# Kernel tuning notes

Hardware: AMD Instinct MI355X
Metric: run time of the kernel (lower is better)

## Reference

```python
import jax, jax.numpy as jnp
import numpy as np

N = 50000
E = 800000
IN_C = 512
HID = 256
OUT_C = 2
NUM_LAYERS = 3
NUM_HIER = 3
EPS = 1e-5


def setup_inputs() -> dict:
    key = jax.random.key(0)
    ks = jax.random.split(key, 24)
    g = lambda k, shp, fan: jax.random.normal(k, shp, jnp.float32) / np.sqrt(fan)
    inp = {
        "x": jax.random.normal(ks[0], (N, IN_C), jnp.float32),
        "edge_index": jax.random.randint(ks[1], (2, E), 0, N, jnp.int64),
        # GCN conv weights/biases
        "conv_w0": g(ks[2], (IN_C, HID), IN_C),
        "conv_ws": g(ks[3], (NUM_LAYERS - 1, HID, HID), HID),
        "conv_b": jnp.zeros((NUM_LAYERS, HID), jnp.float32),
        "bn_g": jnp.ones((NUM_LAYERS, HID), jnp.float32),
        "bn_b": jnp.zeros((NUM_LAYERS, HID), jnp.float32),
        # global-path MLPs
        "fcg_w0": g(ks[4], (HID, HID), HID),
        "fcg_ws": g(ks[5], (NUM_HIER - 1, 2 * HID, HID), 2 * HID),
        "fcg_b": jnp.zeros((NUM_HIER, HID), jnp.float32),
        "bng_g": jnp.ones((NUM_HIER, HID), jnp.float32),
        "bng_b": jnp.zeros((NUM_HIER, HID), jnp.float32),
        # local-path MLPs
        "fcl_w": g(ks[6], (NUM_HIER, HID, HID), HID),
        "fcl_b": jnp.zeros((NUM_HIER, HID), jnp.float32),
        "bnl_g": jnp.ones((NUM_HIER, HID), jnp.float32),
        "bnl_b": jnp.zeros((NUM_HIER, HID), jnp.float32),
        # output heads
        "outg_w": g(ks[7], (HID, OUT_C), HID),
        "outg_b": jnp.zeros((OUT_C,), jnp.float32),
        "outl_w": g(ks[8], (NUM_HIER, HID, OUT_C), HID),
        "outl_b": jnp.zeros((NUM_HIER, OUT_C), jnp.float32),
    }
    return inp


def _gcn_edges(edge_index):
    # add self-loops, compute symmetric normalization D^-1/2 (A+I) D^-1/2
    loops = jnp.arange(N, dtype=edge_index.dtype)
    rows = jnp.concatenate([edge_index[0], loops])
    cols = jnp.concatenate([edge_index[1], loops])
    deg = jax.ops.segment_sum(jnp.ones_like(rows, jnp.float32), rows, num_segments=N)
    dinv = jnp.where(deg > 0, jax.lax.rsqrt(deg), 0.0)
    w = dinv[rows] * dinv[cols]
    return rows, cols, w


def _propagate(h, rows, cols, w):
    msg = h[cols] * w[:, None]          # [E+N, HID] gather
    return jax.ops.segment_sum(msg, rows, num_segments=N)


def _bn(h, gamma, beta):
    m = h.mean(0)
    v = h.var(0)
    return gamma * (h - m) * jax.lax.rsqrt(v + EPS) + beta


def reference(x, edge_index, conv_w0, conv_ws, conv_b, bn_g, bn_b,
              fcg_w0, fcg_ws, fcg_b, bng_g, bng_b,
              fcl_w, fcl_b, bnl_g, bnl_b,
              outg_w, outg_b, outl_w, outl_b):
    rows, cols, ew = _gcn_edges(edge_index)
    h = x
    for i in range(NUM_LAYERS):
        W = conv_w0 if i == 0 else conv_ws[i - 1]
        h = _propagate(h @ W, rows, cols, ew) + conv_b[i]
        h = jax.nn.relu(_bn(h, bn_g[i], bn_b[i]))  # dropout = identity (eval)
    # hierarchical global path
    hg = []
    xg = jax.nn.relu(_bn(h @ fcg_w0 + fcg_b[0], bng_g[0], bng_b[0]))
    hg.append(xg)
    for i in range(NUM_HIER - 1):
        xg = jnp.concatenate([hg[i], h], -1) @ fcg_ws[i] + fcg_b[i + 1]
        xg = jax.nn.relu(_bn(xg, bng_g[i + 1], bng_b[i + 1]))
        hg.append(xg)
    og = jax.nn.log_softmax(hg[-1] @ outg_w + outg_b, axis=-1)
    # local heads
    ol = []
    for i in range(NUM_HIER):
        hl = jax.nn.relu(_bn(hg[i] @ fcl_w[i] + fcl_b[i], bnl_g[i], bnl_b[i]))
        ol.append(jax.nn.log_softmax(hl @ outl_w[i] + outl_b[i], axis=-1))
    # stack: [1 + NUM_HIER, N, OUT_C] (og first, then local heads)
    return jnp.stack([og] + ol, axis=0)
```

## Files before the change

### kernel.cpp

```cpp
#include <hip/hip_runtime.h>
#include <math.h>

#define N_NODES 50000
#define E_EDGES 800000
#define HID 256
#define EPS_BN 1e-5f

typedef __attribute__((ext_vector_type(8))) short short8;
typedef __attribute__((ext_vector_type(4))) float floatx4;
typedef __attribute__((ext_vector_type(8))) unsigned short ushort8v;

__device__ __forceinline__ unsigned short f2bf(float f) {
    unsigned u = __float_as_uint(f);
    u = (u + 0x7FFFu + ((u >> 16) & 1u)) >> 16;
    return (unsigned short)u;
}
__device__ __forceinline__ float bf2f(unsigned short b) {
    return __uint_as_float(((unsigned)b) << 16);
}

__global__ __launch_bounds__(256) void k_deg(const int* __restrict__ rows,
                                             int* __restrict__ deg) {
    int e = blockIdx.x * 256 + threadIdx.x;
    atomicAdd(&deg[rows[e]], 1);
}

__global__ __launch_bounds__(256) void k_dinv(const int* __restrict__ deg,
                                              float* __restrict__ dinv) {
    int n = blockIdx.x * 256 + threadIdx.x;
    if (n < N_NODES) dinv[n] = rsqrtf((float)deg[n] + 1.0f);
}

__global__ __launch_bounds__(1024) void k_scan(const int* __restrict__ deg,
                                               int* __restrict__ rowptr) {
    __shared__ int wsum[16];
    __shared__ int carry_s;
    int tid = threadIdx.x, lane = tid & 63, w = tid >> 6;
    if (tid == 0) carry_s = 0;
    __syncthreads();
    for (int base = 0; base < N_NODES; base += 1024) {
        int v = (base + tid < N_NODES) ? deg[base + tid] : 0;
        int x = v;
#pragma unroll
        for (int d = 1; d < 64; d <<= 1) {
            int t = __shfl_up(x, d);
            if (lane >= d) x += t;
        }
        if (lane == 63) wsum[w] = x;
        __syncthreads();
        if (w == 0) {
            int ws = (lane < 16) ? wsum[lane] : 0;
#pragma unroll
            for (int d = 1; d < 16; d <<= 1) {
                int t = __shfl_up(ws, d);
                if (lane >= d) ws += t;
            }
            if (lane < 16) wsum[lane] = ws;
        }
        __syncthreads();
        int c = carry_s;
        int wbase = (w > 0) ? wsum[w - 1] : 0;
        if (base + tid < N_NODES) rowptr[base + tid] = c + wbase + x - v;
        __syncthreads();
        if (tid == 0) carry_s = c + wsum[15];
        __syncthreads();
    }
    if (threadIdx.x == 0) rowptr[N_NODES] = carry_s;
}

__global__ __launch_bounds__(256) void k_fill(const int* __restrict__ rows,
                                              const int* __restrict__ cols,
                                              const int* __restrict__ rowptr,
                                              int* __restrict__ cursor,
                                              int* __restrict__ colidx) {
    int e = blockIdx.x * 256 + threadIdx.x;
    int r = rows[e];
    int pos = atomicAdd(&cursor[r], 1);
    colidx[rowptr[r] + pos] = cols[e];
}

__global__ __launch_bounds__(256) void k_f2bf_vec(const float* __restrict__ X,
                                                  unsigned short* __restrict__ Y,
                                                  int n4) {
    int i = blockIdx.x * 256 + threadIdx.x;
    if (i >= n4) return;
    float4 v = ((const float4*)X)[i];
    ushort4 o;
    o.x = f2bf(v.x); o.y = f2bf(v.y); o.z = f2bf(v.z); o.w = f2bf(v.w);
    ((ushort4*)Y)[i] = o;
}

__global__ __launch_bounds__(256) void k_wt(const float* __restrict__ W,
                                            unsigned short* __restrict__ Wt,
                                            int K) {
    int idx = blockIdx.x * 256 + threadIdx.x;
    if (idx >= K * HID) return;
    int k = idx >> 8;
    int n = idx & (HID - 1);
    Wt[(size_t)n * K + k] = f2bf(W[idx]);
}

__global__ __launch_bounds__(256) void k_gemm_mfma(
    const unsigned short* __restrict__ A0, int lda0,
    const unsigned short* __restrict__ A1, int lda1, int K0, int K,
    const unsigned short* __restrict__ Bt,
    unsigned short* __restrict__ C,
    const float* __restrict__ rowscale,
    float* __restrict__ stats)
{
    __shared__ alignas(16) unsigned short As[128 * 32];
    __shared__ alignas(16) unsigned short Bs[128 * 32];
    int tid = threadIdx.x;
    int wid = tid >> 6, lane = tid & 63;
    int row0 = blockIdx.x * 128;
    int n0 = blockIdx.y * 128;
    int wrow = (wid & 1) * 64, wcol = (wid >> 1) * 64;
    int lr = lane >> 2;
    int lk = (lane & 3) * 8;
    int qq = lane >> 4, mr = lane & 15;

    floatx4 acc[4][4];
#pragma unroll
    for (int i = 0; i < 4; ++i)
#pragma unroll
        for (int j = 0; j < 4; ++j) {
            floatx4 z = {0.f, 0.f, 0.f, 0.f};
            acc[i][j] = z;
        }

    for (int k0 = 0; k0 < K; k0 += 32) {
        const unsigned short* Abase;
        int lda;
        if (k0 < K0) { Abase = A0 + k0; lda = lda0; }
        else         { Abase = A1 + (k0 - K0); lda = lda1; }
#pragma unroll
        for (int i = 0; i < 2; ++i) {
            int rloc = wid * 32 + i * 16 + lr;
            int grow = row0 + rloc;
            if (grow > N_NODES - 1) grow = N_NODES - 1;
            const unsigned short* g = Abase + (size_t)grow * lda + lk;
            unsigned short* l = As + (wid * 32 + i * 16) * 32;
            __builtin_amdgcn_global_load_lds(
                (const __attribute__((address_space(1))) void*)g,
                (__attribute__((address_space(3))) void*)l, 16, 0, 0);
        }
#pragma unroll
        for (int i = 0; i < 2; ++i) {
            int nloc = wid * 32 + i * 16 + lr;
            const unsigned short* g = Bt + (size_t)(n0 + nloc) * K + k0 + lk;
            unsigned short* l = Bs + (wid * 32 + i * 16) * 32;
            __builtin_amdgcn_global_load_lds(
                (const __attribute__((address_space(1))) void*)g,
                (__attribute__((address_space(3))) void*)l, 16, 0, 0);
        }
        __syncthreads();
        short8 af[4], bfv[4];
#pragma unroll
        for (int i = 0; i < 4; ++i)
            af[i] = *(const short8*)(As + (wrow + i * 16 + mr) * 32 + qq * 8);
#pragma unroll
        for (int j = 0; j < 4; ++j)
            bfv[j] = *(const short8*)(Bs + (wcol + j * 16 + mr) * 32 + qq * 8);
#pragma unroll
        for (int i = 0; i < 4; ++i)
#pragma unroll
            for (int j = 0; j < 4; ++j)
                acc[i][j] = __builtin_amdgcn_mfma_f32_16x16x32_bf16(
                    af[i], bfv[j], acc[i][j], 0, 0, 0);
        __syncthreads();
    }

    float* ls = (float*)As;
    float* lq = ((float*)As) + 128;
    if (stats) {
        ((float*)As)[tid] = 0.f;
        __syncthreads();
    }

    float psum[4] = {0.f, 0.f, 0.f, 0.f};
    float psq[4]  = {0.f, 0.f, 0.f, 0.f};
#pragma unroll
    for (int i = 0; i < 4; ++i) {
        int rbase = row0 + wrow + i * 16 + qq * 4;
#pragma unroll
        for (int r = 0; r < 4; ++r) {
            int row = rbase + r;
            if (row >= N_NODES) continue;
            float rs = rowscale ? rowscale[row] : 1.0f;
            unsigned short* cp = C + (size_t)row * HID + n0 + wcol + mr;
#pragma unroll
            for (int j = 0; j < 4; ++j) {
                float v = acc[i][j][r] * rs;
                cp[j * 16] = f2bf(v);
                psum[j] += v;
                psq[j] += v * v;
            }
        }
    }
    if (stats) {
#pragma unroll
        for (int j = 0; j < 4; ++j) {
            int lc = wcol + j * 16 + mr;
            atomicAdd(&ls[lc], psum[j]);
            atomicAdd(&lq[lc], psq[j]);
        }
        __syncthreads();
        if (tid < 128) atomicAdd(&stats[n0 + tid], ls[tid]);
        else atomicAdd(&stats[HID + n0 + (tid - 128)], lq[tid - 128]);
    }
}

__global__ __launch_bounds__(256) void k_aggregate_bf(
    const unsigned short* __restrict__ g,
    unsigned short* __restrict__ outp,
    const int* __restrict__ rowptr,
    const int* __restrict__ colidx,
    const float* __restrict__ dinv,
    float* __restrict__ stats) {
    int lane = threadIdx.x & 63;
    int gw = blockIdx.x * 4 + (threadIdx.x >> 6);
    int totw = gridDim.x * 4;
    float s0 = 0.f, s1 = 0.f, s2 = 0.f, s3 = 0.f;
    float q0 = 0.f, q1 = 0.f, q2 = 0.f, q3 = 0.f;
    for (int node = gw; node < N_NODES; node += totw) {
        int s = rowptr[node], e = rowptr[node + 1];
        ushort4 sv = ((const ushort4*)(g + (size_t)node * HID))[lane];
        float a0 = bf2f(sv.x), a1 = bf2f(sv.y), a2 = bf2f(sv.z), a3 = bf2f(sv.w);
        for (int base = s; base < e; base += 64) {
            int cnt = e - base; if (cnt > 64) cnt = 64;
            int cidx = (lane < cnt) ? colidx[base + lane] : 0;
            int j = 0;
            for (; j + 4 <= cnt; j += 4) {
                int c0 = __shfl(cidx, j + 0), c1 = __shfl(cidx, j + 1);
                int c2 = __shfl(cidx, j + 2), c3 = __shfl(cidx, j + 3);
                ushort4 v0 = ((const ushort4*)(g + (size_t)c0 * HID))[lane];
                ushort4 v1 = ((const ushort4*)(g + (size_t)c1 * HID))[lane];
                ushort4 v2 = ((const ushort4*)(g + (size_t)c2 * HID))[lane];
                ushort4 v3 = ((const ushort4*)(g + (size_t)c3 * HID))[lane];
                a0 += (bf2f(v0.x) + bf2f(v1.x)) + (bf2f(v2.x) + bf2f(v3.x));
                a1 += (bf2f(v0.y) + bf2f(v1.y)) + (bf2f(v2.y) + bf2f(v3.y));
                a2 += (bf2f(v0.z) + bf2f(v1.z)) + (bf2f(v2.z) + bf2f(v3.z));
                a3 += (bf2f(v0.w) + bf2f(v1.w)) + (bf2f(v2.w) + bf2f(v3.w));
            }
            for (; j < cnt; ++j) {
                int c = __shfl(cidx, j);
                ushort4 v = ((const ushort4*)(g + (size_t)c * HID))[lane];
                a0 += bf2f(v.x); a1 += bf2f(v.y); a2 += bf2f(v.z); a3 += bf2f(v.w);
            }
        }
        float rs = dinv[node];
        a0 *= rs; a1 *= rs; a2 *= rs; a3 *= rs;
        ushort4 o;
        o.x = f2bf(a0); o.y = f2bf(a1); o.z = f2bf(a2); o.w = f2bf(a3);
        ((ushort4*)(outp + (size_t)node * HID))[lane] = o;
        s0 += a0; s1 += a1; s2 += a2; s3 += a3;
        q0 += a0 * a0; q1 += a1 * a1; q2 += a2 * a2; q3 += a3 * a3;
    }
    __shared__ float ls[HID], lq[HID];
    ls[threadIdx.x] = 0.f; lq[threadIdx.x] = 0.f;
    __syncthreads();
    atomicAdd(&ls[lane * 4 + 0], s0); atomicAdd(&lq[lane * 4 + 0], q0);
    atomicAdd(&ls[lane * 4 + 1], s1); atomicAdd(&lq[lane * 4 + 1], q1);
    atomicAdd(&ls[lane * 4 + 2], s2); atomicAdd(&lq[lane * 4 + 2], q2);
    atomicAdd(&ls[lane * 4 + 3], s3); atomicAdd(&lq[lane * 4 + 3], q3);
    __syncthreads();
    atomicAdd(&stats[threadIdx.x], ls[threadIdx.x]);
    atomicAdd(&stats[HID + threadIdx.x], lq[threadIdx.x]);
}

__global__ __launch_bounds__(256) void k_bnfinal(const float* __restrict__ stats,
                                                 const float* __restrict__ gamma,
                                                 const float* __restrict__ beta,
                                                 float* __restrict__ scsh) {
    int ch = threadIdx.x;
    const float invn = 1.0f / (float)N_NODES;
    float mean = stats[ch] * invn;
    float var = stats[HID + ch] * invn - mean * mean;
    var = fmaxf(var, 0.f);
    float sc = gamma[ch] * rsqrtf(var + EPS_BN);
    scsh[ch] = sc;
    scsh[HID + ch] = beta[ch] - mean * sc;
}

__global__ __launch_bounds__(256) void k_bnapply_bf(const unsigned short* __restrict__ X,
                                                    unsigned short* __restrict__ Y,
                                                    const float* __restrict__ scsh) {
    int i = blockIdx.x * 256 + threadIdx.x;
    int ch8 = (i & 31) * 8;
    ushort8v v = *(const ushort8v*)(X + (size_t)i * 8);
    ushort8v o;
#pragma unroll
    for (int k = 0; k < 8; ++k) {
        float f = bf2f((unsigned short)v[k]);
        o[k] = f2bf(fmaxf(f * scsh[ch8 + k] + scsh[HID + ch8 + k], 0.f));
    }
    *(ushort8v*)(Y + (size_t)i * 8) = o;
}

__global__ __launch_bounds__(256) void k_head_bf(const unsigned short* __restrict__ H,
                                                 const float* __restrict__ W,
                                                 const float* __restrict__ b,
                                                 float* __restrict__ outp) {
    int wave = (blockIdx.x * 256 + threadIdx.x) >> 6;
    int lane = threadIdx.x & 63;
    if (wave >= N_NODES) return;
    ushort4 h4 = ((const ushort4*)(H + (size_t)wave * HID))[lane];
    float h0 = bf2f(h4.x), h1 = bf2f(h4.y), h2 = bf2f(h4.z), h3 = bf2f(h4.w);
    const float2* W2 = (const float2*)W;
    float2 w0 = W2[lane * 4 + 0], w1 = W2[lane * 4 + 1];
    float2 w2 = W2[lane * 4 + 2], w3 = W2[lane * 4 + 3];
    float p0 = h0 * w0.x + h1 * w1.x + h2 * w2.x + h3 * w3.x;
    float p1 = h0 * w0.y + h1 * w1.y + h2 * w2.y + h3 * w3.y;
    for (int off = 32; off > 0; off >>= 1) {
        p0 += __shfl_down(p0, off);
        p1 += __shfl_down(p1, off);
    }
    if (lane == 0) {
        float z0 = p0 + b[0], z1 = p1 + b[1];
        float m = fmaxf(z0, z1);
        float lse = m + logf(expf(z0 - m) + expf(z1 - m));
        outp[(size_t)wave * 2 + 0] = z0 - lse;
        outp[(size_t)wave * 2 + 1] = z1 - lse;
    }
}

extern "C" void kernel_launch(void* const* d_in, const int* in_sizes, int n_in,
                              void* d_out, int out_size, void* d_ws, size_t ws_size,
                              hipStream_t stream) {
    const float* x       = (const float*)d_in[0];
    const int*   ei      = (const int*)d_in[1];
    const float* conv_w0 = (const float*)d_in[2];
    const float* conv_ws = (const float*)d_in[3];
    const float* bn_g    = (const float*)d_in[5];
    const float* bn_b    = (const float*)d_in[6];
    const float* fcg_w0  = (const float*)d_in[7];
    const float* fcg_ws  = (const float*)d_in[8];
    const float* bng_g   = (const float*)d_in[10];
    const float* bng_b   = (const float*)d_in[11];
    const float* fcl_w   = (const float*)d_in[12];
    const float* bnl_g   = (const float*)d_in[14];
    const float* bnl_b   = (const float*)d_in[15];
    const float* outg_w  = (const float*)d_in[16];
    const float* outg_b  = (const float*)d_in[17];
    const float* outl_w  = (const float*)d_in[18];
    const float* outl_b  = (const float*)d_in[19];
    float* out = (float*)d_out;

    const int* rows = ei;
    const int* cols = ei + E_EDGES;

    char* ws = (char*)d_ws;
    size_t off = 0;
    auto carve = [&](size_t bytes) -> void* {
        void* p = ws + off;
        off = (off + bytes + 255) & ~(size_t)255;
        return p;
    };
    const size_t ACT = (size_t)N_NODES * HID * 2;
    unsigned short* xbf = (unsigned short*)carve((size_t)N_NODES * 512 * 2);
    unsigned short* tG  = (unsigned short*)carve(ACT);
    unsigned short* tA  = (unsigned short*)carve(ACT);
    unsigned short* hbf = (unsigned short*)carve(ACT);
    unsigned short* g1  = (unsigned short*)carve(ACT);
    unsigned short* g2  = (unsigned short*)carve(ACT);
    unsigned short* hl  = (unsigned short*)carve(ACT);
    unsigned short* wt_conv0 = (unsigned short*)carve(256 * 512 * 2);
    unsigned short* wt_conv1 = (unsigned short*)carve(256 * 256 * 2);
    unsigned short* wt_conv2 = (unsigned short*)carve(256 * 256 * 2);
    unsigned short* wt_fcg0  = (unsigned short*)carve(256 * 256 * 2);
    unsigned short* wt_fcgs0 = (unsigned short*)carve(256 * 512 * 2);
    unsigned short* wt_fcgs1 = (unsigned short*)carve(256 * 512 * 2);
    unsigned short* wt_fcl0  = (unsigned short*)carve(256 * 256 * 2);
    unsigned short* wt_fcl1  = (unsigned short*)carve(256 * 256 * 2);
    unsigned short* wt_fcl2  = (unsigned short*)carve(256 * 256 * 2);
    int*   deg    = (int*)carve(2 * 50048 * 4);
    int*   cursor = deg + 50048;
    int*   rowptr = (int*)carve((size_t)(N_NODES + 1) * 4);
    float* dinv   = (float*)carve((size_t)N_NODES * 4);
    int*   colidx = (int*)carve((size_t)E_EDGES * 4);
    float* stats_all = (float*)carve(9 * 2 * HID * 4);
    float* scsh   = (float*)carve(2 * HID * 4);
    (void)off; (void)ws_size; (void)in_sizes; (void)n_in; (void)out_size;

    hipMemsetAsync(deg, 0, 2 * 50048 * 4, stream);
    hipMemsetAsync(stats_all, 0, 9 * 2 * HID * 4, stream);
    k_deg<<<E_EDGES / 256, 256, 0, stream>>>(rows, deg);
    k_dinv<<<(N_NODES + 255) / 256, 256, 0, stream>>>(deg, dinv);
    k_scan<<<1, 1024, 0, stream>>>(deg, rowptr);
    k_fill<<<E_EDGES / 256, 256, 0, stream>>>(rows, cols, rowptr, cursor, colidx);

    k_f2bf_vec<<<(N_NODES * 512 / 4 + 255) / 256, 256, 0, stream>>>(x, xbf, N_NODES * 512 / 4);
    k_wt<<<(512 * 256 + 255) / 256, 256, 0, stream>>>(conv_w0, wt_conv0, 512);
    k_wt<<<(256 * 256 + 255) / 256, 256, 0, stream>>>(conv_ws, wt_conv1, 256);
    k_wt<<<(256 * 256 + 255) / 256, 256, 0, stream>>>(conv_ws + 65536, wt_conv2, 256);
    k_wt<<<(256 * 256 + 255) / 256, 256, 0, stream>>>(fcg_w0, wt_fcg0, 256);
    k_wt<<<(512 * 256 + 255) / 256, 256, 0, stream>>>(fcg_ws, wt_fcgs0, 512);
    k_wt<<<(512 * 256 + 255) / 256, 256, 0, stream>>>(fcg_ws + 131072, wt_fcgs1, 512);
    k_wt<<<(256 * 256 + 255) / 256, 256, 0, stream>>>(fcl_w, wt_fcl0, 256);
    k_wt<<<(256 * 256 + 255) / 256, 256, 0, stream>>>(fcl_w + 65536, wt_fcl1, 256);
    k_wt<<<(256 * 256 + 255) / 256, 256, 0, stream>>>(fcl_w + 131072, wt_fcl2, 256);

    dim3 ggrid((N_NODES + 127) / 128, 2);
    auto gemm = [&](const unsigned short* A0, int lda0,
                    const unsigned short* A1, int lda1, int K0, int K,
                    const unsigned short* Bt, unsigned short* C,
                    const float* rs, float* st) {
        k_gemm_mfma<<<ggrid, 256, 0, stream>>>(A0, lda0, A1, lda1, K0, K, Bt, C, rs, st);
    };
    auto bnfin = [&](float* st, const unsigned short* X, unsigned short* Y,
                     const float* gamma, const float* beta) {
        k_bnfinal<<<1, 256, 0, stream>>>(st, gamma, beta, scsh);
        k_bnapply_bf<<<N_NODES * 32 / 256, 256, 0, stream>>>(X, Y, scsh);
    };
    auto agg = [&](const unsigned short* in, unsigned short* outb, float* st) {
        k_aggregate_bf<<<782, 256, 0, stream>>>(in, outb, rowptr, colidx, dinv, st);
    };
    float* st;

    st = stats_all + 0 * 512;
    gemm(xbf, 512, nullptr, 0, 512, 512, wt_conv0, tG, dinv, nullptr);
    agg(tG, tA, st);
    bnfin(st, tA, g1, bn_g + 0, bn_b + 0);
    st = stats_all + 1 * 512;
    gemm(g1, 256, nullptr, 0, 256, 256, wt_conv1, tG, dinv, nullptr);
    agg(tG, tA, st);
    bnfin(st, tA, g2, bn_g + 256, bn_b + 256);
    st = stats_all + 2 * 512;
    gemm(g2, 256, nullptr, 0, 256, 256, wt_conv2, tG, dinv, nullptr);
    agg(tG, tA, st);
    bnfin(st, tA, hbf, bn_g + 512, bn_b + 512);

    st = stats_all + 3 * 512;
    gemm(hbf, 256, nullptr, 0, 256, 256, wt_fcg0, tG, nullptr, st);
    bnfin(st, tG, g1, bng_g + 0, bng_b + 0);
    st = stats_all + 4 * 512;
    gemm(g1, 256, nullptr, 0, 256, 256, wt_fcl0, tG, nullptr, st);
    bnfin(st, tG, hl, bnl_g + 0, bnl_b + 0);
    k_head_bf<<<N_NODES / 4, 256, 0, stream>>>(hl, outl_w, outl_b,
                                               out + (size_t)1 * N_NODES * 2);
    st = stats_all + 5 * 512;
    gemm(g1, 256, hbf, 256, 256, 512, wt_fcgs0, tG, nullptr, st);
    bnfin(st, tG, g2, bng_g + 256, bng_b + 256);
    st = stats_all + 6 * 512;
    gemm(g2, 256, nullptr, 0, 256, 256, wt_fcl1, tG, nullptr, st);
    bnfin(st, tG, hl, bnl_g + 256, bnl_b + 256);
    k_head_bf<<<N_NODES / 4, 256, 0, stream>>>(hl, outl_w + 512, outl_b + 2,
                                               out + (size_t)2 * N_NODES * 2);
    st = stats_all + 7 * 512;
    gemm(g2, 256, hbf, 256, 256, 512, wt_fcgs1, tG, nullptr, st);
    bnfin(st, tG, g1, bng_g + 512, bng_b + 512);
    st = stats_all + 8 * 512;
    gemm(g1, 256, nullptr, 0, 256, 256, wt_fcl2, tG, nullptr, st);
    bnfin(st, tG, hl, bnl_g + 512, bnl_b + 512);
    k_head_bf<<<N_NODES / 4, 256, 0, stream>>>(hl, outl_w + 1024, outl_b + 4,
                                               out + (size_t)3 * N_NODES * 2);
    k_head_bf<<<N_NODES / 4, 256, 0, stream>>>(g1, outg_w, outg_b, out);
}
```

Before: 1.085 ms.

## Split aggregation wave into half-wave edge groups and fuse local BN into heads

The aggregation kernel now has each half-wave process alternate neighbors using 16-byte loads of 8 channels per lane. The two halves are combined with a cross-lane xor shuffle, and the grid grows from 782 to 2048 blocks. The three local-head BN-apply passes are dropped: the head kernel now applies the BN scale/shift and ReLU itself from the GEMM output, which removes a full activation write and read per head. This adds an extra shuffle reduction per node, and only half the lanes do the final store.

```diff
diff --git a/kernel.cpp b/kernel.cpp
--- a/kernel.cpp
+++ b/kernel.cpp
@@ -217,55 +217,82 @@
     const int* __restrict__ colidx,
     const float* __restrict__ dinv,
     float* __restrict__ stats) {
-    int lane = threadIdx.x & 63;
-    int gw = blockIdx.x * 4 + (threadIdx.x >> 6);
+    int tid = threadIdx.x;
+    int lane = tid & 63;
+    int half = lane >> 5;
+    int hl = lane & 31;
+    int gw = blockIdx.x * 4 + (tid >> 6);
     int totw = gridDim.x * 4;
-    float s0 = 0.f, s1 = 0.f, s2 = 0.f, s3 = 0.f;
-    float q0 = 0.f, q1 = 0.f, q2 = 0.f, q3 = 0.f;
+    int srcBase = half << 5;
+    float sacc[8] = {0.f, 0.f, 0.f, 0.f, 0.f, 0.f, 0.f, 0.f};
+    float qacc[8] = {0.f, 0.f, 0.f, 0.f, 0.f, 0.f, 0.f, 0.f};
+
     for (int node = gw; node < N_NODES; node += totw) {
         int s = rowptr[node], e = rowptr[node + 1];
-        ushort4 sv = ((const ushort4*)(g + (size_t)node * HID))[lane];
-        float a0 = bf2f(sv.x), a1 = bf2f(sv.y), a2 = bf2f(sv.z), a3 = bf2f(sv.w);
-        for (int base = s; base < e; base += 64) {
-            int cnt = e - base; if (cnt > 64) cnt = 64;
-            int cidx = (lane < cnt) ? colidx[base + lane] : 0;
-            int j = 0;
-            for (; j + 4 <= cnt; j += 4) {
-                int c0 = __shfl(cidx, j + 0), c1 = __shfl(cidx, j + 1);
-                int c2 = __shfl(cidx, j + 2), c3 = __shfl(cidx, j + 3);
-                ushort4 v0 = ((const ushort4*)(g + (size_t)c0 * HID))[lane];
-                ushort4 v1 = ((const ushort4*)(g + (size_t)c1 * HID))[lane];
-                ushort4 v2 = ((const ushort4*)(g + (size_t)c2 * HID))[lane];
-                ushort4 v3 = ((const ushort4*)(g + (size_t)c3 * HID))[lane];
-                a0 += (bf2f(v0.x) + bf2f(v1.x)) + (bf2f(v2.x) + bf2f(v3.x));
-                a1 += (bf2f(v0.y) + bf2f(v1.y)) + (bf2f(v2.y) + bf2f(v3.y));
-                a2 += (bf2f(v0.z) + bf2f(v1.z)) + (bf2f(v2.z) + bf2f(v3.z));
-                a3 += (bf2f(v0.w) + bf2f(v1.w)) + (bf2f(v2.w) + bf2f(v3.w));
+        int degn = e - s;
+        float a[8];
+        if (half) {
+            ushort8v sv = ((const ushort8v*)(g + (size_t)node * HID))[hl];
+#pragma unroll
+            for (int k = 0; k < 8; ++k) a[k] = bf2f(sv[k]);
+        } else {
+#pragma unroll
+            for (int k = 0; k < 8; ++k) a[k] = 0.f;
+        }
+        for (int base = 0; base < degn; base += 64) {
+            int cnt = degn - base; if (cnt > 64) cnt = 64;
+            int cidx = (lane < cnt) ? colidx[s + base + lane] : 0;
+            int mycidx = __shfl(cidx, 2 * hl + half);
+            int myCnt = (cnt - half + 1) >> 1;
+            int t = 0;
+            for (; t + 4 <= myCnt; t += 4) {
+                int c0 = __shfl(mycidx, srcBase + t + 0);
+                int c1 = __shfl(mycidx, srcBase + t + 1);
+                int c2 = __shfl(mycidx, srcBase + t + 2);
+                int c3 = __shfl(mycidx, srcBase + t + 3);
+                ushort8v v0 = ((const ushort8v*)(g + (size_t)c0 * HID))[hl];
+                ushort8v v1 = ((const ushort8v*)(g + (size_t)c1 * HID))[hl];
+                ushort8v v2 = ((const ushort8v*)(g + (size_t)c2 * HID))[hl];
+                ushort8v v3 = ((const ushort8v*)(g + (size_t)c3 * HID))[hl];
+#pragma unroll
+                for (int k = 0; k < 8; ++k)
+                    a[k] += (bf2f(v0[k]) + bf2f(v1[k])) + (bf2f(v2[k]) + bf2f(v3[k]));
             }
-            for (; j < cnt; ++j) {
-                int c = __shfl(cidx, j);
-                ushort4 v = ((const ushort4*)(g + (size_t)c * HID))[lane];
-                a0 += bf2f(v.x); a1 += bf2f(v.y); a2 += bf2f(v.z); a3 += bf2f(v.w);
+            for (; t < myCnt; ++t) {
+                int c = __shfl(mycidx, srcBase + t);
+                ushort8v v = ((const ushort8v*)(g + (size_t)c * HID))[hl];
+#pragma unroll
+                for (int k = 0; k < 8; ++k) a[k] += bf2f(v[k]);
             }
         }
-        float rs = dinv[node];
-        a0 *= rs; a1 *= rs; a2 *= rs; a3 *= rs;
-        ushort4 o;
-        o.x = f2bf(a0); o.y = f2bf(a1); o.z = f2bf(a2); o.w = f2bf(a3);
-        ((ushort4*)(outp + (size_t)node * HID))[lane] = o;
-        s0 += a0; s1 += a1; s2 += a2; s3 += a3;
-        q0 += a0 * a0; q1 += a1 * a1; q2 += a2 * a2; q3 += a3 * a3;
+#pragma unroll
+        for (int k = 0; k < 8; ++k) a[k] += __shfl_xor(a[k], 32);
+        if (!half) {
+            float rs = dinv[node];
+            ushort8v o;
+#pragma unroll
+            for (int k = 0; k < 8; ++k) {
+                float val = a[k] * rs;
+                o[k] = f2bf(val);
+                sacc[k] += val;
+                qacc[k] += val * val;
+            }
+            ((ushort8v*)(outp + (size_t)node * HID))[hl] = o;
+        }
     }
     __shared__ float ls[HID], lq[HID];
-    ls[threadIdx.x] = 0.f; lq[threadIdx.x] = 0.f;
+    ls[tid] = 0.f; lq[tid] = 0.f;
     __syncthreads();
-    atomicAdd(&ls[lane * 4 + 0], s0); atomicAdd(&lq[lane * 4 + 0], q0);
-    atomicAdd(&ls[lane * 4 + 1], s1); atomicAdd(&lq[lane * 4 + 1], q1);
-    atomicAdd(&ls[lane * 4 + 2], s2); atomicAdd(&lq[lane * 4 + 2], q2);
-    atomicAdd(&ls[lane * 4 + 3], s3); atomicAdd(&lq[lane * 4 + 3], q3);
+    if (!half) {
+#pragma unroll
+        for (int k = 0; k < 8; ++k) {
+            atomicAdd(&ls[hl * 8 + k], sacc[k]);
+            atomicAdd(&lq[hl * 8 + k], qacc[k]);
+        }
+    }
     __syncthreads();
-    atomicAdd(&stats[threadIdx.x], ls[threadIdx.x]);
-    atomicAdd(&stats[HID + threadIdx.x], lq[threadIdx.x]);
+    atomicAdd(&stats[tid], ls[tid]);
+    atomicAdd(&stats[HID + tid], lq[tid]);
 }
 
 __global__ __launch_bounds__(256) void k_bnfinal(const float* __restrict__ stats,
@@ -298,6 +325,7 @@
 }
 
 __global__ __launch_bounds__(256) void k_head_bf(const unsigned short* __restrict__ H,
+                                                 const float* __restrict__ scsh,
                                                  const float* __restrict__ W,
                                                  const float* __restrict__ b,
                                                  float* __restrict__ outp) {
@@ -306,6 +334,13 @@
     if (wave >= N_NODES) return;
     ushort4 h4 = ((const ushort4*)(H + (size_t)wave * HID))[lane];
     float h0 = bf2f(h4.x), h1 = bf2f(h4.y), h2 = bf2f(h4.z), h3 = bf2f(h4.w);
+    if (scsh) {
+        int ch = lane * 4;
+        h0 = fmaxf(h0 * scsh[ch + 0] + scsh[HID + ch + 0], 0.f);
+        h1 = fmaxf(h1 * scsh[ch + 1] + scsh[HID + ch + 1], 0.f);
+        h2 = fmaxf(h2 * scsh[ch + 2] + scsh[HID + ch + 2], 0.f);
+        h3 = fmaxf(h3 * scsh[ch + 3] + scsh[HID + ch + 3], 0.f);
+    }
     const float2* W2 = (const float2*)W;
     float2 w0 = W2[lane * 4 + 0], w1 = W2[lane * 4 + 1];
     float2 w2 = W2[lane * 4 + 2], w3 = W2[lane * 4 + 3];
@@ -363,7 +398,6 @@
     unsigned short* hbf = (unsigned short*)carve(ACT);
     unsigned short* g1  = (unsigned short*)carve(ACT);
     unsigned short* g2  = (unsigned short*)carve(ACT);
-    unsigned short* hl  = (unsigned short*)carve(ACT);
     unsigned short* wt_conv0 = (unsigned short*)carve(256 * 512 * 2);
     unsigned short* wt_conv1 = (unsigned short*)carve(256 * 256 * 2);
     unsigned short* wt_conv2 = (unsigned short*)carve(256 * 256 * 2);
@@ -413,7 +447,7 @@
         k_bnapply_bf<<<N_NODES * 32 / 256, 256, 0, stream>>>(X, Y, scsh);
     };
     auto agg = [&](const unsigned short* in, unsigned short* outb, float* st) {
-        k_aggregate_bf<<<782, 256, 0, stream>>>(in, outb, rowptr, colidx, dinv, st);
+        k_aggregate_bf<<<2048, 256, 0, stream>>>(in, outb, rowptr, colidx, dinv, st);
     };
     float* st;
 
@@ -435,24 +469,24 @@
     bnfin(st, tG, g1, bng_g + 0, bng_b + 0);
     st = stats_all + 4 * 512;
     gemm(g1, 256, nullptr, 0, 256, 256, wt_fcl0, tG, nullptr, st);
-    bnfin(st, tG, hl, bnl_g + 0, bnl_b + 0);
-    k_head_bf<<<N_NODES / 4, 256, 0, stream>>>(hl, outl_w, outl_b,
+    k_bnfinal<<<1, 256, 0, stream>>>(st, bnl_g + 0, bnl_b + 0, scsh);
+    k_head_bf<<<N_NODES / 4, 256, 0, stream>>>(tG, scsh, outl_w, outl_b,
                                                out + (size_t)1 * N_NODES * 2);
     st = stats_all + 5 * 512;
     gemm(g1, 256, hbf, 256, 256, 512, wt_fcgs0, tG, nullptr, st);
     bnfin(st, tG, g2, bng_g + 256, bng_b + 256);
     st = stats_all + 6 * 512;
     gemm(g2, 256, nullptr, 0, 256, 256, wt_fcl1, tG, nullptr, st);
-    bnfin(st, tG, hl, bnl_g + 256, bnl_b + 256);
-    k_head_bf<<<N_NODES / 4, 256, 0, stream>>>(hl, outl_w + 512, outl_b + 2,
+    k_bnfinal<<<1, 256, 0, stream>>>(st, bnl_g + 256, bnl_b + 256, scsh);
+    k_head_bf<<<N_NODES / 4, 256, 0, stream>>>(tG, scsh, outl_w + 512, outl_b + 2,
                                                out + (size_t)2 * N_NODES * 2);
     st = stats_all + 7 * 512;
     gemm(g2, 256, hbf, 256, 256, 512, wt_fcgs1, tG, nullptr, st);
     bnfin(st, tG, g1, bng_g + 512, bng_b + 512);
     st = stats_all + 8 * 512;
     gemm(g1, 256, nullptr, 0, 256, 256, wt_fcl2, tG, nullptr, st);
-    bnfin(st, tG, hl, bnl_g + 512, bnl_b + 512);
-    k_head_bf<<<N_NODES / 4, 256, 0, stream>>>(hl, outl_w + 1024, outl_b + 4,
+    k_bnfinal<<<1, 256, 0, stream>>>(st, bnl_g + 512, bnl_b + 512, scsh);
+    k_head_bf<<<N_NODES / 4, 256, 0, stream>>>(tG, scsh, outl_w + 1024, outl_b + 4,
                                                out + (size_t)3 * N_NODES * 2);
-    k_head_bf<<<N_NODES / 4, 256, 0, stream>>>(g1, outg_w, outg_b, out);
-}
+    k_head_bf<<<N_NODES / 4, 256, 0, stream>>>(g1, nullptr, outg_w, outg_b, out);
+}
```

Result: slower. 1.119 ms (+3.2%).

## Fold BN finalize into apply kernels and fuse local-head BN into head

Applied to the files above, without the earlier changes.

Removes the single-block BN finalize kernel and has every thread recompute scale/shift from the raw stats inside the apply kernel. The three local-head BN+ReLU passes are now applied inside the head kernel, which drops three full activation write/read round trips and several launches. The cost is redundant rsqrt/stat loads per element, which should be cheap and cached.

```diff
diff --git a/kernel.cpp b/kernel.cpp
--- a/kernel.cpp
+++ b/kernel.cpp
@@ -17,6 +17,16 @@
 }
 __device__ __forceinline__ float bf2f(unsigned short b) {
     return __uint_as_float(((unsigned)b) << 16);
+}
+__device__ __forceinline__ void bn_scsh(const float* stats, const float* gamma,
+                                        const float* beta, int ch,
+                                        float& sc, float& sh) {
+    const float invn = 1.0f / (float)N_NODES;
+    float mean = stats[ch] * invn;
+    float var = stats[HID + ch] * invn - mean * mean;
+    var = fmaxf(var, 0.f);
+    sc = gamma[ch] * rsqrtf(var + EPS_BN);
+    sh = beta[ch] - mean * sc;
 }
 
 __global__ __launch_bounds__(256) void k_deg(const int* __restrict__ rows,
@@ -268,36 +278,29 @@
     atomicAdd(&stats[HID + threadIdx.x], lq[threadIdx.x]);
 }
 
-__global__ __launch_bounds__(256) void k_bnfinal(const float* __restrict__ stats,
-                                                 const float* __restrict__ gamma,
-                                                 const float* __restrict__ beta,
-                                                 float* __restrict__ scsh) {
-    int ch = threadIdx.x;
-    const float invn = 1.0f / (float)N_NODES;
-    float mean = stats[ch] * invn;
-    float var = stats[HID + ch] * invn - mean * mean;
-    var = fmaxf(var, 0.f);
-    float sc = gamma[ch] * rsqrtf(var + EPS_BN);
-    scsh[ch] = sc;
-    scsh[HID + ch] = beta[ch] - mean * sc;
-}
-
 __global__ __launch_bounds__(256) void k_bnapply_bf(const unsigned short* __restrict__ X,
                                                     unsigned short* __restrict__ Y,
-                                                    const float* __restrict__ scsh) {
+                                                    const float* __restrict__ stats,
+                                                    const float* __restrict__ gamma,
+                                                    const float* __restrict__ beta) {
     int i = blockIdx.x * 256 + threadIdx.x;
     int ch8 = (i & 31) * 8;
     ushort8v v = *(const ushort8v*)(X + (size_t)i * 8);
     ushort8v o;
 #pragma unroll
     for (int k = 0; k < 8; ++k) {
+        float sc, sh;
+        bn_scsh(stats, gamma, beta, ch8 + k, sc, sh);
         float f = bf2f((unsigned short)v[k]);
-        o[k] = f2bf(fmaxf(f * scsh[ch8 + k] + scsh[HID + ch8 + k], 0.f));
+        o[k] = f2bf(fmaxf(f * sc + sh, 0.f));
     }
     *(ushort8v*)(Y + (size_t)i * 8) = o;
 }
 
 __global__ __launch_bounds__(256) void k_head_bf(const unsigned short* __restrict__ H,
+                                                 const float* __restrict__ stats,
+                                                 const float* __restrict__ gamma,
+                                                 const float* __restrict__ beta,
                                                  const float* __restrict__ W,
                                                  const float* __restrict__ b,
                                                  float* __restrict__ outp) {
@@ -306,6 +309,14 @@
     if (wave >= N_NODES) return;
     ushort4 h4 = ((const ushort4*)(H + (size_t)wave * HID))[lane];
     float h0 = bf2f(h4.x), h1 = bf2f(h4.y), h2 = bf2f(h4.z), h3 = bf2f(h4.w);
+    if (stats) {
+        int ch = lane * 4;
+        float sc, sh;
+        bn_scsh(stats, gamma, beta, ch + 0, sc, sh); h0 = fmaxf(h0 * sc + sh, 0.f);
+        bn_scsh(stats, gamma, beta, ch + 1, sc, sh); h1 = fmaxf(h1 * sc + sh, 0.f);
+        bn_scsh(stats, gamma, beta, ch + 2, sc, sh); h2 = fmaxf(h2 * sc + sh, 0.f);
+        bn_scsh(stats, gamma, beta, ch + 3, sc, sh); h3 = fmaxf(h3 * sc + sh, 0.f);
+    }
     const float2* W2 = (const float2*)W;
     float2 w0 = W2[lane * 4 + 0], w1 = W2[lane * 4 + 1];
     float2 w2 = W2[lane * 4 + 2], w3 = W2[lane * 4 + 3];
@@ -363,7 +374,6 @@
     unsigned short* hbf = (unsigned short*)carve(ACT);
     unsigned short* g1  = (unsigned short*)carve(ACT);
     unsigned short* g2  = (unsigned short*)carve(ACT);
-    unsigned short* hl  = (unsigned short*)carve(ACT);
     unsigned short* wt_conv0 = (unsigned short*)carve(256 * 512 * 2);
     unsigned short* wt_conv1 = (unsigned short*)carve(256 * 256 * 2);
     unsigned short* wt_conv2 = (unsigned short*)carve(256 * 256 * 2);
@@ -379,7 +389,6 @@
     float* dinv   = (float*)carve((size_t)N_NODES * 4);
     int*   colidx = (int*)carve((size_t)E_EDGES * 4);
     float* stats_all = (float*)carve(9 * 2 * HID * 4);
-    float* scsh   = (float*)carve(2 * HID * 4);
     (void)off; (void)ws_size; (void)in_sizes; (void)n_in; (void)out_size;
 
     hipMemsetAsync(deg, 0, 2 * 50048 * 4, stream);
@@ -407,10 +416,9 @@
                     const float* rs, float* st) {
         k_gemm_mfma<<<ggrid, 256, 0, stream>>>(A0, lda0, A1, lda1, K0, K, Bt, C, rs, st);
     };
-    auto bnfin = [&](float* st, const unsigned short* X, unsigned short* Y,
-                     const float* gamma, const float* beta) {
-        k_bnfinal<<<1, 256, 0, stream>>>(st, gamma, beta, scsh);
-        k_bnapply_bf<<<N_NODES * 32 / 256, 256, 0, stream>>>(X, Y, scsh);
+    auto bnapply = [&](float* st, const unsigned short* X, unsigned short* Y,
+                       const float* gamma, const float* beta) {
+        k_bnapply_bf<<<N_NODES * 32 / 256, 256, 0, stream>>>(X, Y, st, gamma, beta);
     };
     auto agg = [&](const unsigned short* in, unsigned short* outb, float* st) {
         k_aggregate_bf<<<782, 256, 0, stream>>>(in, outb, rowptr, colidx, dinv, st);
@@ -420,39 +428,40 @@
     st = stats_all + 0 * 512;
     gemm(xbf, 512, nullptr, 0, 512, 512, wt_conv0, tG, dinv, nullptr);
     agg(tG, tA, st);
-    bnfin(st, tA, g1, bn_g + 0, bn_b + 0);
+    bnapply(st, tA, g1, bn_g + 0, bn_b + 0);
     st = stats_all + 1 * 512;
     gemm(g1, 256, nullptr, 0, 256, 256, wt_conv1, tG, dinv, nullptr);
     agg(tG, tA, st);
-    bnfin(st, tA, g2, bn_g + 256, bn_b + 256);
+    bnapply(st, tA, g2, bn_g + 256, bn_b + 256);
     st = stats_all + 2 * 512;
     gemm(g2, 256, nullptr, 0, 256, 256, wt_conv2, tG, dinv, nullptr);
     agg(tG, tA, st);
-    bnfin(st, tA, hbf, bn_g + 512, bn_b + 512);
+    bnapply(st, tA, hbf, bn_g + 512, bn_b + 512);
 
     st = stats_all + 3 * 512;
     gemm(hbf, 256, nullptr, 0, 256, 256, wt_fcg0, tG, nullptr, st);
-    bnfin(st, tG, g1, bng_g + 0, bng_b + 0);
+    bnapply(st, tG, g1, bng_g + 0, bng_b + 0);
     st = stats_all + 4 * 512;
     gemm(g1, 256, nullptr, 0, 256, 256, wt_fcl0, tG, nullptr, st);
-    bnfin(st, tG, hl, bnl_g + 0, bnl_b + 0);
-    k_head_bf<<<N_NODES / 4, 256, 0, stream>>>(hl, outl_w, outl_b,
+    k_head_bf<<<N_NODES / 4, 256, 0, stream>>>(tG, st, bnl_g + 0, bnl_b + 0,
+                                               outl_w, outl_b,
                                                out + (size_t)1 * N_NODES * 2);
     st = stats_all + 5 * 512;
     gemm(g1, 256, hbf, 256, 256, 512, wt_fcgs0, tG, nullptr, st);
-    bnfin(st, tG, g2, bng_g + 256, bng_b + 256);
+    bnapply(st, tG, g2, bng_g + 256, bng_b + 256);
     st = stats_all + 6 * 512;
     gemm(g2, 256, nullptr, 0, 256, 256, wt_fcl1, tG, nullptr, st);
-    bnfin(st, tG, hl, bnl_g + 256, bnl_b + 256);
-    k_head_bf<<<N_NODES / 4, 256, 0, stream>>>(hl, outl_w + 512, outl_b + 2,
+    k_head_bf<<<N_NODES / 4, 256, 0, stream>>>(tG, st, bnl_g + 256, bnl_b + 256,
+                                               outl_w + 512, outl_b + 2,
                                                out + (size_t)2 * N_NODES * 2);
     st = stats_all + 7 * 512;
     gemm(g2, 256, hbf, 256, 256, 512, wt_fcgs1, tG, nullptr, st);
-    bnfin(st, tG, g1, bng_g + 512, bng_b + 512);
+    bnapply(st, tG, g1, bng_g + 512, bng_b + 512);
     st = stats_all + 8 * 512;
     gemm(g1, 256, nullptr, 0, 256, 256, wt_fcl2, tG, nullptr, st);
-    bnfin(st, tG, hl, bnl_g + 512, bnl_b + 512);
-    k_head_bf<<<N_NODES / 4, 256, 0, stream>>>(hl, outl_w + 1024, outl_b + 4,
+    k_head_bf<<<N_NODES / 4, 256, 0, stream>>>(tG, st, bnl_g + 512, bnl_b + 512,
+                                               outl_w + 1024, outl_b + 4,
                                                out + (size_t)3 * N_NODES * 2);
-    k_head_bf<<<N_NODES / 4, 256, 0, stream>>>(g1, outg_w, outg_b, out);
-}
+    k_head_bf<<<N_NODES / 4, 256, 0, stream>>>(g1, nullptr, nullptr, nullptr,
+                                               outg_w, outg_b, out);
+}
```

Result: no change. 1.072 ms (-1.2%).
